# Kernel tuning notes

Hardware: AMD Instinct MI355X
Metric: run time of the kernel (lower is better)

The kernel has to match this reference:

```python
import jax, jax.numpy as jnp
import numpy as np

NP_, NA, NPR = 3000, 25, 1071
N = NP_ + NA + NPR          # 4096 total nodes
D = 256                     # latent_dim
H = 8                       # num_heads
DH = D // H                 # head dim 32
FF = 4 * D                  # feed-forward dim
BLOCKS = 3                  # args.block_num
E = 131072                  # edges = N * 32 avg degree
EPS = 1e-5


def setup_inputs() -> dict:
    key = jax.random.key(0)
    ks = jax.random.split(key, 16)
    s = 1.0 / np.sqrt(D)
    return {
        "adj_row": jax.random.randint(ks[0], (E,), 0, N, dtype=jnp.int32),
        "adj_col": jax.random.randint(ks[1], (E,), 0, N, dtype=jnp.int32),
        "adj_val": jax.random.uniform(ks[2], (E,), dtype=jnp.float32),
        "pe": jax.random.normal(ks[3], (NP_, D), dtype=jnp.float32) * s,
        "ae": jax.random.normal(ks[4], (NA, D), dtype=jnp.float32) * s,
        "qe": jax.random.normal(ks[5], (NPR, D), dtype=jnp.float32) * s,
        "Wqkv": jax.random.normal(ks[6], (D, 3 * D), dtype=jnp.float32) * s,
        "Wo": jax.random.normal(ks[7], (D, D), dtype=jnp.float32) * s,
        "W1": jax.random.normal(ks[8], (D, FF), dtype=jnp.float32) * s,
        "b1": jnp.zeros((FF,), dtype=jnp.float32),
        "W2": jax.random.normal(ks[9], (FF, D), dtype=jnp.float32) * (1.0 / np.sqrt(FF)),
        "b2": jnp.zeros((D,), dtype=jnp.float32),
        "ln1_g": jnp.ones((D,), dtype=jnp.float32),
        "ln1_b": jnp.zeros((D,), dtype=jnp.float32),
        "ln2_g": jnp.ones((D,), dtype=jnp.float32),
        "ln2_b": jnp.zeros((D,), dtype=jnp.float32),
    }


def _layer_norm(x, g, b):
    m = jnp.mean(x, axis=-1, keepdims=True)
    v = jnp.mean(jnp.square(x - m), axis=-1, keepdims=True)
    return (x - m) * jax.lax.rsqrt(v + EPS) * g + b


def _encoder_layer(x, Wqkv, Wo, W1, b1, W2, b2, ln1_g, ln1_b, ln2_g, ln2_b):
    # x: [N, D]; standard post-LN transformer encoder (dropout = 0)
    qkv = x @ Wqkv                                   # [N, 3D]
    q, k, v = jnp.split(qkv, 3, axis=-1)
    q = q.reshape(N, H, DH)
    k = k.reshape(N, H, DH)
    v = v.reshape(N, H, DH)
    scores = jnp.einsum("nhd,mhd->hnm", q, k) / np.sqrt(DH)  # [H, N, N]
    att = jax.nn.softmax(scores, axis=-1)
    o = jnp.einsum("hnm,mhd->nhd", att, v).reshape(N, D) @ Wo
    x = _layer_norm(x + o, ln1_g, ln1_b)
    h = jax.nn.relu(x @ W1 + b1) @ W2 + b2
    return _layer_norm(x + h, ln2_g, ln2_b)


def _spmm(adj_row, adj_col, adj_val, x):
    # sparse [N,N] @ dense [N,D] via gather + segment-sum scatter
    msgs = adj_val[:, None] * x[adj_col]             # [E, D]
    return jax.ops.segment_sum(msgs, adj_row, num_segments=N)


def reference(adj_row, adj_col, adj_val, pe, ae, qe, Wqkv, Wo, W1, b1, W2, b2,
              ln1_g, ln1_b, ln2_g, ln2_b):
    cur = jnp.concatenate([pe, ae, qe], axis=0)      # [N, D]
    total = cur
    for _ in range(BLOCKS):
        t = _spmm(adj_row, adj_col, adj_val, cur)
        t = _encoder_layer(t, Wqkv, Wo, W1, b1, W2, b2, ln1_g, ln1_b, ln2_g, ln2_b)
        cur = t + cur                                # residual per block
        total = total + cur                          # sum over embeds list
    protein = total[:NP_]
    aa = total[NP_:NP_ + NA]
    prop = total[NP_ + NA:]
    return total, protein, aa, prop
```

## Files before the change

### kernel.cpp

```cpp
#include <hip/hip_runtime.h>
#include <hip/hip_bf16.h>


#define NPROT 3000
#define NAA   25
#define NPROP 1071
#define NTOT  4096
#define DIM   256
#define NH    8
#define DHD   32
#define FFD   1024
#define NEDGE 131072
#define LNEPS 1e-5f
#define KSPLIT 4
#define KVQ (NTOT/KSPLIT)

typedef unsigned short u16;
typedef unsigned int u32;
typedef __attribute__((ext_vector_type(8))) short short8v;
typedef __attribute__((ext_vector_type(4))) float float4v;
typedef __attribute__((ext_vector_type(2))) unsigned int uint2v;

__device__ __forceinline__ u16 f2bu(float x){
  union { __hip_bfloat16 h; u16 u; } c; c.h = __float2bfloat16(x); return c.u;
}
__device__ __forceinline__ float bu2f(u16 u){
  union { u32 i; float f; } c; c.i = ((u32)u) << 16; return c.f;
}
__device__ __forceinline__ float4v mfma16(short8v a, short8v b, float4v c){
  return __builtin_amdgcn_mfma_f32_16x16x32_bf16(a, b, c, 0, 0, 0);
}
__device__ __forceinline__ u32 packbf(float lo, float hi){
  u32 ul = __builtin_bit_cast(u32, lo);
  u32 uh = __builtin_bit_cast(u32, hi);
  return (ul >> 16) | (uh & 0xFFFF0000u);
}
__device__ __forceinline__ void gload_lds16(const u16* g, u16* l){
  __builtin_amdgcn_global_load_lds(
      (const __attribute__((address_space(1))) void*)g,
      (__attribute__((address_space(3))) void*)l, 16, 0, 0);
}

__global__ __launch_bounds__(256) void k_embed(const float* __restrict__ pe, const float* __restrict__ ae,
                                               const float* __restrict__ qe,
                                               float* __restrict__ cur, float* __restrict__ tot,
                                               u16* __restrict__ curb){
  int i = blockIdx.x*256 + threadIdx.x;
  int row = i >> 8;
  float v;
  if (row < NPROT)           v = pe[i];
  else if (row < NPROT+NAA)  v = ae[i - NPROT*DIM];
  else                       v = qe[i - (NPROT+NAA)*DIM];
  cur[i] = v; tot[i] = v; curb[i] = f2bu(v);
}

__global__ __launch_bounds__(256) void k_zero(int* __restrict__ p, int n){
  int i = blockIdx.x*256 + threadIdx.x; if (i < n) p[i] = 0;
}

__global__ __launch_bounds__(256) void k_wconv_all(const float* __restrict__ Wqkv, const float* __restrict__ Wo,
                                                   const float* __restrict__ W1, const float* __restrict__ W2,
                                                   u16* __restrict__ wqkvt, u16* __restrict__ wot,
                                                   u16* __restrict__ w1t, u16* __restrict__ w2t){
  int b = blockIdx.x;
  const float* W; u16* Wt; int K, N, n;
  if (b < 768)       { W = Wqkv; Wt = wqkvt; K = 256;  N = 768;  n = b; }
  else if (b < 1024) { W = Wo;   Wt = wot;   K = 256;  N = 256;  n = b - 768; }
  else if (b < 2048) { W = W1;   Wt = w1t;   K = 256;  N = 1024; n = b - 1024; }
  else               { W = W2;   Wt = w2t;   K = 1024; N = 256;  n = b - 2048; }
  for (int k = threadIdx.x; k < K; k += 256)
    Wt[(size_t)n*K + k] = f2bu(W[(size_t)k*N + n]);
}

__global__ __launch_bounds__(256) void k_hist(const int* __restrict__ rows, int* __restrict__ cnt){
  int e = blockIdx.x*256 + threadIdx.x; if (e < NEDGE) atomicAdd(&cnt[rows[e]], 1);
}

__global__ __launch_bounds__(64) void k_scan(const int* __restrict__ cnt, int* __restrict__ rowptr,
                                             int* __restrict__ cursor){
  int lane = threadIdx.x;
  int sum = 0;
  for (int i = 0; i < 64; ++i) sum += cnt[lane*64 + i];
  int pref = sum;
  #pragma unroll
  for (int off = 1; off < 64; off <<= 1){
    int u = __shfl_up(pref, off);
    if (lane >= off) pref += u;
  }
  int run = pref - sum;
  for (int i = 0; i < 64; ++i){
    int c = cnt[lane*64 + i];
    rowptr[lane*64 + i] = run;
    cursor[lane*64 + i] = run;
    run += c;
  }
  if (lane == 63) rowptr[NTOT] = run;
}

__global__ __launch_bounds__(256) void k_scatter(const int* __restrict__ rows, const int* __restrict__ cols,
                                                 const float* __restrict__ vals, int* __restrict__ cursor,
                                                 int* __restrict__ ccol, float* __restrict__ cval){
  int e = blockIdx.x*256 + threadIdx.x; if (e >= NEDGE) return;
  int p = atomicAdd(&cursor[rows[e]], 1);
  ccol[p] = cols[e]; cval[p] = vals[e];
}

__global__ __launch_bounds__(256) void k_spmm(const int* __restrict__ rowptr, const int* __restrict__ ccol,
                                              const float* __restrict__ cval, const u16* __restrict__ xb,
                                              float* __restrict__ out, u16* __restrict__ outb){
  int r = blockIdx.x, c = threadIdx.x;
  int s = rowptr[r], e = rowptr[r+1];
  float acc = 0.f;
  for (int i = s; i < e; ++i)
    acc += cval[i] * bu2f(xb[((size_t)ccol[i] << 8) + c]);
  out[((size_t)r << 8) + c] = acc;
  outb[((size_t)r << 8) + c] = f2bu(acc);
}

template<int RELU, int BIAS, int BF16OUT>
__global__ __launch_bounds__(256) void k_gemm64(const u16* __restrict__ A, const u16* __restrict__ Wt,
                                                const float* __restrict__ bias, void* __restrict__ Cv,
                                                int M, int K, int Nc){
  __shared__ u16 Al[64*64];
  __shared__ u16 Bl[64*64];
  const int tid = threadIdx.x;
  const int w  = tid >> 6, l = tid & 63, lr = l & 15, g = l >> 4;
  const int row0 = blockIdx.y*64, col0 = blockIdx.x*64;
  const int wm = (w >> 1)*32, wn = (w & 1)*32;
  const int srow = (l >> 3);
  const int soct = (l & 7) ^ srow;
  float4v acc[2][2] = {};

  for (int k0 = 0; k0 < K; k0 += 64){
    #pragma unroll
    for (int i = 0; i < 2; ++i){
      int row = 16*w + 8*i + srow;
      gload_lds16(A  + (size_t)(row0 + row)*K + k0 + soct*8, Al + (16*w + 8*i)*64);
      gload_lds16(Wt + (size_t)(col0 + row)*K + k0 + soct*8, Bl + (16*w + 8*i)*64);
    }
    __syncthreads();
    #pragma unroll
    for (int kk = 0; kk < 2; ++kk){
      short8v af[2], bfr[2];
      #pragma unroll
      for (int i = 0; i < 2; ++i){
        int am = wm + 16*i + lr;
        af[i]  = *(const short8v*)(Al + am*64 + (((4*kk + g) ^ (am & 7))*8));
        int bn = wn + 16*i + lr;
        bfr[i] = *(const short8v*)(Bl + bn*64 + (((4*kk + g) ^ (bn & 7))*8));
      }
      acc[0][0] = mfma16(af[0], bfr[0], acc[0][0]);
      acc[0][1] = mfma16(af[0], bfr[1], acc[0][1]);
      acc[1][0] = mfma16(af[1], bfr[0], acc[1][0]);
      acc[1][1] = mfma16(af[1], bfr[1], acc[1][1]);
    }
    __syncthreads();
  }

  #pragma unroll
  for (int mi = 0; mi < 2; ++mi){
    #pragma unroll
    for (int ni = 0; ni < 2; ++ni){
      int col = col0 + wn + 16*ni + lr;
      float bv = BIAS ? bias[col] : 0.f;
      #pragma unroll
      for (int j = 0; j < 4; ++j){
        int row = row0 + wm + 16*mi + 4*g + j;
        float v = acc[mi][ni][j] + bv;
        if (RELU) v = fmaxf(v, 0.f);
        if (BF16OUT) ((u16*)Cv)[(size_t)row*Nc + col] = f2bu(v);
        else         ((float*)Cv)[(size_t)row*Nc + col] = v;
      }
    }
  }
}

__global__ __launch_bounds__(256) void k_attn_mfma(const u16* __restrict__ qbf,
                                                   u16* __restrict__ p0, u16* __restrict__ p1,
                                                   u16* __restrict__ p2, u16* __restrict__ p3,
                                                   float* __restrict__ mbuf, float* __restrict__ lbuf){
  __shared__ u16 Vt[2][32*64];
  __shared__ u16 Pl[4][16*64];
  __shared__ float Fl[4][16];
  const int h   = blockIdx.y;
  const int ks  = blockIdx.z;
  const int qb  = blockIdx.x * 128;
  const int tid = threadIdx.x;
  const int w   = tid >> 6;
  const int l   = tid & 63;
  const int lr  = l & 15;
  const int g   = l >> 4;
  const int sr  = tid >> 2;
  const int sq  = tid & 3;
  const float SC  = 0.17677669529663687f;
  const float SCL = 0.25503837f;
  const float DEFER = 31.368f;
  u16* opart = (ks == 0) ? p0 : (ks == 1) ? p1 : (ks == 2) ? p2 : p3;

  short8v qfA = *(const short8v*)(qbf + (size_t)(qb + 16*w + lr)*768 + h*DHD + 8*g);
  short8v qfB = *(const short8v*)(qbf + (size_t)(qb + 64 + 16*w + lr)*768 + h*DHD + 8*g);
  short8v ones;
  #pragma unroll
  for (int j = 0; j < 8; ++j) ones[j] = (short)0x3F80;

  float4v oaA0 = {0,0,0,0}, oaA1 = {0,0,0,0}, acclA = {0,0,0,0};
  float4v oaB0 = {0,0,0,0}, oaB1 = {0,0,0,0}, acclB = {0,0,0,0};
  float mrunA = -1e30f, mrunB = -1e30f;
  u16* pw = &Pl[w][0];

  const u16* vp = qbf + (size_t)(ks*KVQ + sr)*768 + 512 + h*DHD + 8*sq;
  const u16* kp = qbf + (size_t)(ks*KVQ + lr)*768 + 256 + h*DHD + 8*g;
  short8v vreg = *(const short8v*)vp;
  short8v kf0 = *(const short8v*)(kp);
  short8v kf1 = *(const short8v*)(kp + (size_t)16*768);
  short8v kf2 = *(const short8v*)(kp + (size_t)32*768);
  short8v kf3 = *(const short8v*)(kp + (size_t)48*768);

  const int gh = g >> 1, gl = 4*(g & 1);
  const int slotp0 = (0 + g) ^ (lr & 7);
  const int slotp1 = (4 + g) ^ (lr & 7);

  const int NIT = KVQ/64;
  for (int t = 0; t < NIT; ++t){
    u16* vt = &Vt[t & 1][0];
    #pragma unroll
    for (int j = 0; j < 8; ++j){
      int row  = 8*sq + j;
      int slot = (sr >> 3) ^ j;
      vt[row*64 + slot*8 + (sr & 7)] = (u16)vreg[j];
    }
    __syncthreads();
    vp += (size_t)64*768;
    vreg = *(const short8v*)vp;

    float4v sA0 = mfma16(kf0, qfA, (float4v){0,0,0,0});
    float4v sA1 = mfma16(kf1, qfA, (float4v){0,0,0,0});
    float4v sA2 = mfma16(kf2, qfA, (float4v){0,0,0,0});
    float4v sA3 = mfma16(kf3, qfA, (float4v){0,0,0,0});
    float4v sB0 = mfma16(kf0, qfB, (float4v){0,0,0,0});
    float4v sB1 = mfma16(kf1, qfB, (float4v){0,0,0,0});
    float4v sB2 = mfma16(kf2, qfB, (float4v){0,0,0,0});
    float4v sB3 = mfma16(kf3, qfB, (float4v){0,0,0,0});
    kp += (size_t)64*768;
    kf0 = *(const short8v*)(kp);
    kf1 = *(const short8v*)(kp + (size_t)16*768);
    kf2 = *(const short8v*)(kp + (size_t)32*768);
    kf3 = *(const short8v*)(kp + (size_t)48*768);

    short8v v00 = *(const short8v*)(vt + lr*64      + slotp0*8);
    short8v v10 = *(const short8v*)(vt + (lr+16)*64 + slotp0*8);
    short8v v01 = *(const short8v*)(vt + lr*64      + slotp1*8);
    short8v v11 = *(const short8v*)(vt + (lr+16)*64 + slotp1*8);

    {
      float m0 = fmaxf(fmaxf(fmaxf(sA0[0],sA0[1]),sA0[2]),sA0[3]);
      float m1 = fmaxf(fmaxf(fmaxf(sA1[0],sA1[1]),sA1[2]),sA1[3]);
      float m2 = fmaxf(fmaxf(fmaxf(sA2[0],sA2[1]),sA2[2]),sA2[3]);
      float m3 = fmaxf(fmaxf(fmaxf(sA3[0],sA3[1]),sA3[2]),sA3[3]);
      float tm = fmaxf(fmaxf(fmaxf(m0,m1),m2),m3);
      tm = fmaxf(tm, __shfl_xor(tm, 16));
      tm = fmaxf(tm, __shfl_xor(tm, 32));
      const bool nomax = __all(tm <= mrunA + DEFER);
      float fac = 1.f;
      if (!nomax){
        float mn = fmaxf(mrunA, tm);
        fac = exp2f((mrunA - mn)*SCL);
        mrunA = mn;
      }
      float mns = mrunA*SCL;
      #pragma unroll
      for (int j = 0; j < 4; ++j){
        sA0[j] = exp2f(__builtin_fmaf(sA0[j], SCL, -mns));
        sA1[j] = exp2f(__builtin_fmaf(sA1[j], SCL, -mns));
        sA2[j] = exp2f(__builtin_fmaf(sA2[j], SCL, -mns));
        sA3[j] = exp2f(__builtin_fmaf(sA3[j], SCL, -mns));
      }
      uint2v* d0 = (uint2v*)(pw + lr*64 + ((0 + gh) ^ (lr & 7))*8 + gl);
      uint2v* d1 = (uint2v*)(pw + lr*64 + ((2 + gh) ^ (lr & 7))*8 + gl);
      uint2v* d2 = (uint2v*)(pw + lr*64 + ((4 + gh) ^ (lr & 7))*8 + gl);
      uint2v* d3 = (uint2v*)(pw + lr*64 + ((6 + gh) ^ (lr & 7))*8 + gl);
      *d0 = (uint2v){packbf(sA0[0],sA0[1]), packbf(sA0[2],sA0[3])};
      *d1 = (uint2v){packbf(sA1[0],sA1[1]), packbf(sA1[2],sA1[3])};
      *d2 = (uint2v){packbf(sA2[0],sA2[1]), packbf(sA2[2],sA2[3])};
      *d3 = (uint2v){packbf(sA3[0],sA3[1]), packbf(sA3[2],sA3[3])};
      if (!nomax){
        if (g == 0) Fl[w][lr] = fac;
        float fq0 = Fl[w][4*g+0], fq1 = Fl[w][4*g+1], fq2 = Fl[w][4*g+2], fq3 = Fl[w][4*g+3];
        oaA0[0]*=fq0; oaA0[1]*=fq1; oaA0[2]*=fq2; oaA0[3]*=fq3;
        oaA1[0]*=fq0; oaA1[1]*=fq1; oaA1[2]*=fq2; oaA1[3]*=fq3;
        acclA[0]*=fq0; acclA[1]*=fq1; acclA[2]*=fq2; acclA[3]*=fq3;
      }
      short8v pa0 = *(const short8v*)(pw + lr*64 + slotp0*8);
      short8v pa1 = *(const short8v*)(pw + lr*64 + slotp1*8);
      oaA0  = mfma16(pa0, v00, oaA0);
      oaA1  = mfma16(pa0, v10, oaA1);
      acclA = mfma16(pa0, ones, acclA);
      oaA0  = mfma16(pa1, v01, oaA0);
      oaA1  = mfma16(pa1, v11, oaA1);
      acclA = mfma16(pa1, ones, acclA);
    }
    {
      float m0 = fmaxf(fmaxf(fmaxf(sB0[0],sB0[1]),sB0[2]),sB0[3]);
      float m1 = fmaxf(fmaxf(fmaxf(sB1[0],sB1[1]),sB1[2]),sB1[3]);
      float m2 = fmaxf(fmaxf(fmaxf(sB2[0],sB2[1]),sB2[2]),sB2[3]);
      float m3 = fmaxf(fmaxf(fmaxf(sB3[0],sB3[1]),sB3[2]),sB3[3]);
      float tm = fmaxf(fmaxf(fmaxf(m0,m1),m2),m3);
      tm = fmaxf(tm, __shfl_xor(tm, 16));
      tm = fmaxf(tm, __shfl_xor(tm, 32));
      const bool nomax = __all(tm <= mrunB + DEFER);
      float fac = 1.f;
      if (!nomax){
        float mn = fmaxf(mrunB, tm);
        fac = exp2f((mrunB - mn)*SCL);
        mrunB = mn;
      }
      float mns = mrunB*SCL;
      #pragma unroll
      for (int j = 0; j < 4; ++j){
        sB0[j] = exp2f(__builtin_fmaf(sB0[j], SCL, -mns));
        sB1[j] = exp2f(__builtin_fmaf(sB1[j], SCL, -mns));
        sB2[j] = exp2f(__builtin_fmaf(sB2[j], SCL, -mns));
        sB3[j] = exp2f(__builtin_fmaf(sB3[j], SCL, -mns));
      }
      uint2v* d0 = (uint2v*)(pw + lr*64 + ((0 + gh) ^ (lr & 7))*8 + gl);
      uint2v* d1 = (uint2v*)(pw + lr*64 + ((2 + gh) ^ (lr & 7))*8 + gl);
      uint2v* d2 = (uint2v*)(pw + lr*64 + ((4 + gh) ^ (lr & 7))*8 + gl);
      uint2v* d3 = (uint2v*)(pw + lr*64 + ((6 + gh) ^ (lr & 7))*8 + gl);
      *d0 = (uint2v){packbf(sB0[0],sB0[1]), packbf(sB0[2],sB0[3])};
      *d1 = (uint2v){packbf(sB1[0],sB1[1]), packbf(sB1[2],sB1[3])};
      *d2 = (uint2v){packbf(sB2[0],sB2[1]), packbf(sB2[2],sB2[3])};
      *d3 = (uint2v){packbf(sB3[0],sB3[1]), packbf(sB3[2],sB3[3])};
      if (!nomax){
        if (g == 0) Fl[w][lr] = fac;
        float fq0 = Fl[w][4*g+0], fq1 = Fl[w][4*g+1], fq2 = Fl[w][4*g+2], fq3 = Fl[w][4*g+3];
        oaB0[0]*=fq0; oaB0[1]*=fq1; oaB0[2]*=fq2; oaB0[3]*=fq3;
        oaB1[0]*=fq0; oaB1[1]*=fq1; oaB1[2]*=fq2; oaB1[3]*=fq3;
        acclB[0]*=fq0; acclB[1]*=fq1; acclB[2]*=fq2; acclB[3]*=fq3;
      }
      short8v pa0 = *(const short8v*)(pw + lr*64 + slotp0*8);
      short8v pa1 = *(const short8v*)(pw + lr*64 + slotp1*8);
      oaB0  = mfma16(pa0, v00, oaB0);
      oaB1  = mfma16(pa0, v10, oaB1);
      acclB = mfma16(pa0, ones, acclB);
      oaB0  = mfma16(pa1, v01, oaB0);
      oaB1  = mfma16(pa1, v11, oaB1);
      acclB = mfma16(pa1, ones, acclB);
    }
  }

  #pragma unroll
  for (int j = 0; j < 4; ++j){
    size_t rowA = (size_t)(qb + 16*w + 4*g + j);
    size_t rowB = rowA + 64;
    opart[rowA*DIM + h*DHD + lr]      = f2bu(oaA0[j]);
    opart[rowA*DIM + h*DHD + 16 + lr] = f2bu(oaA1[j]);
    opart[rowB*DIM + h*DHD + lr]      = f2bu(oaB0[j]);
    opart[rowB*DIM + h*DHD + 16 + lr] = f2bu(oaB1[j]);
  }
  if (l < 16){
    size_t miA = (size_t)(ks*NH + h)*NTOT + qb + 16*w + lr;
    mbuf[miA]      = mrunA*SC;
    mbuf[miA + 64] = mrunB*SC;
  }
  if (lr == 0){
    #pragma unroll
    for (int j = 0; j < 4; ++j){
      size_t miA = (size_t)(ks*NH + h)*NTOT + qb + 16*w + 4*g + j;
      lbuf[miA]      = acclA[j];
      lbuf[miA + 64] = acclB[j];
    }
  }
}

__global__ __launch_bounds__(256) void k_attn_merge4(const u16* __restrict__ p0, const u16* __restrict__ p1,
                                                     const u16* __restrict__ p2, const u16* __restrict__ p3,
                                                     const float* __restrict__ mbuf, const float* __restrict__ lbuf,
                                                     u16* __restrict__ obf){
  int i = blockIdx.x*256 + threadIdx.x;
  int r = i >> 8, c = i & 255, h = c >> 5;
  float m0 = mbuf[(size_t)(0*NH + h)*NTOT + r];
  float m1 = mbuf[(size_t)(1*NH + h)*NTOT + r];
  float m2 = mbuf[(size_t)(2*NH + h)*NTOT + r];
  float m3 = mbuf[(size_t)(3*NH + h)*NTOT + r];
  float M = fmaxf(fmaxf(m0, m1), fmaxf(m2, m3));
  float e0 = __expf(m0 - M), e1 = __expf(m1 - M);
  float e2 = __expf(m2 - M), e3 = __expf(m3 - M);
  float L = e0*lbuf[(size_t)(0*NH + h)*NTOT + r] + e1*lbuf[(size_t)(1*NH + h)*NTOT + r]
          + e2*lbuf[(size_t)(2*NH + h)*NTOT + r] + e3*lbuf[(size_t)(3*NH + h)*NTOT + r];
  float acc = e0*bu2f(p0[i]) + e1*bu2f(p1[i]) + e2*bu2f(p2[i]) + e3*bu2f(p3[i]);
  obf[i] = f2bu(acc / L);
}

template<int DUAL>
__global__ __launch_bounds__(256) void k_add_ln(const float* __restrict__ a, const float* __restrict__ b,
                                                const float* __restrict__ g, const float* __restrict__ be,
                                                float* __restrict__ out, u16* __restrict__ out2){
  __shared__ float red[4];
  int r = blockIdx.x, c = threadIdx.x;
  float v = a[((size_t)r << 8) + c] + b[((size_t)r << 8) + c];
  float s = v;
  #pragma unroll
  for (int off = 32; off; off >>= 1) s += __shfl_down(s, off);
  if ((c & 63) == 0) red[c >> 6] = s;
  __syncthreads();
  float mean = (red[0]+red[1]+red[2]+red[3]) * (1.f/DIM);
  __syncthreads();
  float d = v - mean;
  float s2 = d*d;
  #pragma unroll
  for (int off = 32; off; off >>= 1) s2 += __shfl_down(s2, off);
  if ((c & 63) == 0) red[c >> 6] = s2;
  __syncthreads();
  float var = (red[0]+red[1]+red[2]+red[3]) * (1.f/DIM);
  float rv = d * rsqrtf(var + LNEPS) * g[c] + be[c];
  out[((size_t)r << 8) + c] = rv;
  if (DUAL) out2[((size_t)r << 8) + c] = f2bu(rv);
}

template<int FINAL>
__global__ __launch_bounds__(256) void k_add_ln_upd(const float* __restrict__ a, const float* __restrict__ b,
                                                    const float* __restrict__ g, const float* __restrict__ be,
                                                    float* __restrict__ cur, float* __restrict__ tot,
                                                    u16* __restrict__ curb, float* __restrict__ out){
  __shared__ float red[4];
  int r = blockIdx.x, c = threadIdx.x;
  size_t idx = ((size_t)r << 8) + c;
  float v = a[idx] + b[idx];
  float s = v;
  #pragma unroll
  for (int off = 32; off; off >>= 1) s += __shfl_down(s, off);
  if ((c & 63) == 0) red[c >> 6] = s;
  __syncthreads();
  float mean = (red[0]+red[1]+red[2]+red[3]) * (1.f/DIM);
  __syncthreads();
  float d = v - mean;
  float s2 = d*d;
  #pragma unroll
  for (int off = 32; off; off >>= 1) s2 += __shfl_down(s2, off);
  if ((c & 63) == 0) red[c >> 6] = s2;
  __syncthreads();
  float var = (red[0]+red[1]+red[2]+red[3]) * (1.f/DIM);
  float rv = d * rsqrtf(var + LNEPS) * g[c] + be[c];
  float cu = cur[idx] + rv;
  cur[idx] = cu;
  if (!FINAL) curb[idx] = f2bu(cu);
  float tv = tot[idx] + cu;
  tot[idx] = tv;
  if (FINAL){
    out[idx] = tv;
    out[(size_t)NTOT*DIM + idx] = tv;
  }
}

extern "C" void kernel_launch(void* const* d_in, const int* in_sizes, int n_in,
                              void* d_out, int out_size, void* d_ws, size_t ws_size,
                              hipStream_t stream){
  const int*   adj_row = (const int*)  d_in[0];
  const int*   adj_col = (const int*)  d_in[1];
  const float* adj_val = (const float*)d_in[2];
  const float* pe   = (const float*)d_in[3];
  const float* ae   = (const float*)d_in[4];
  const float* qe   = (const float*)d_in[5];
  const float* Wqkv = (const float*)d_in[6];
  const float* Wo   = (const float*)d_in[7];
  const float* W1   = (const float*)d_in[8];
  const float* b1   = (const float*)d_in[9];
  const float* W2   = (const float*)d_in[10];
  const float* b2   = (const float*)d_in[11];
  const float* g1   = (const float*)d_in[12];
  const float* be1  = (const float*)d_in[13];
  const float* g2   = (const float*)d_in[14];
  const float* be2  = (const float*)d_in[15];
  float* out = (float*)d_out;

  char* w = (char*)d_ws;
  float* cur  = (float*)w; w += (size_t)NTOT*DIM*4;
  float* tot  = (float*)w; w += (size_t)NTOT*DIM*4;
  float* tf   = (float*)w; w += (size_t)NTOT*DIM*4;
  float* pbuf = (float*)w; w += (size_t)NTOT*DIM*4;
  float* x1   = (float*)w; w += (size_t)NTOT*DIM*4;
  u16* tbf    = (u16*)w;   w += (size_t)NTOT*DIM*2;
  u16* curb   = (u16*)w;   w += (size_t)NTOT*DIM*2;
  u16* x1b    = (u16*)w;   w += (size_t)NTOT*DIM*2;
  u16* hq     = (u16*)w;   w += (size_t)NTOT*FFD*2;
  u16* wqkvt  = (u16*)w;   w += (size_t)768*256*2;
  u16* wot    = (u16*)w;   w += (size_t)256*256*2;
  u16* w1t    = (u16*)w;   w += (size_t)1024*256*2;
  u16* w2t    = (u16*)w;   w += (size_t)256*1024*2;
  int* rowptr = (int*)w;   w += (size_t)(NTOT+1)*4;
  int* cnt    = (int*)w;   w += (size_t)NTOT*4;
  int* cursor = (int*)w;   w += (size_t)NTOT*4;
  int* ccol   = (int*)w;   w += (size_t)NEDGE*4;
  float* cval = (float*)w; w += (size_t)NEDGE*4;
  u16* qbf = hq;
  u16* obf = hq;
  u16* pp0 = (u16*)x1;
  u16* pp1 = (u16*)x1 + (size_t)NTOT*DIM;
  u16* pp2 = x1b;
  u16* pp3 = curb;
  float* mbuf = (float*)tbf;
  float* lbuf = mbuf + (size_t)KSPLIT*NH*NTOT;

  k_zero<<<16, 256, 0, stream>>>(cnt, NTOT);
  k_embed<<<NTOT, 256, 0, stream>>>(pe, ae, qe, cur, tot, curb);
  k_hist<<<NEDGE/256, 256, 0, stream>>>(adj_row, cnt);
  k_scan<<<1, 64, 0, stream>>>(cnt, rowptr, cursor);
  k_scatter<<<NEDGE/256, 256, 0, stream>>>(adj_row, adj_col, adj_val, cursor, ccol, cval);
  k_wconv_all<<<2304, 256, 0, stream>>>(Wqkv, Wo, W1, W2, wqkvt, wot, w1t, w2t);

  for (int blk = 0; blk < 3; ++blk){
    k_spmm<<<NTOT, 256, 0, stream>>>(rowptr, ccol, cval, curb, tf, tbf);
    k_gemm64<0,0,1><<<dim3(768/64, NTOT/64), 256, 0, stream>>>(tbf, wqkvt, nullptr, qbf, NTOT, 256, 768);
    k_attn_mfma<<<dim3(NTOT/128, NH, KSPLIT), 256, 0, stream>>>(qbf, pp0, pp1, pp2, pp3, mbuf, lbuf);
    k_attn_merge4<<<NTOT*DIM/256, 256, 0, stream>>>(pp0, pp1, pp2, pp3, mbuf, lbuf, obf);
    k_gemm64<0,0,0><<<dim3(256/64, NTOT/64), 256, 0, stream>>>(obf, wot, nullptr, pbuf, NTOT, 256, 256);
    k_add_ln<1><<<NTOT, 256, 0, stream>>>(tf, pbuf, g1, be1, x1, x1b);
    k_gemm64<1,1,1><<<dim3(1024/64, NTOT/64), 256, 0, stream>>>(x1b, w1t, b1, hq, NTOT, 256, 1024);
    k_gemm64<0,1,0><<<dim3(256/64, NTOT/64), 256, 0, stream>>>(hq, w2t, b2, pbuf, NTOT, 1024, 256);
    if (blk < 2)
      k_add_ln_upd<0><<<NTOT, 256, 0, stream>>>(x1, pbuf, g2, be2, cur, tot, curb, nullptr);
    else
      k_add_ln_upd<1><<<NTOT, 256, 0, stream>>>(x1, pbuf, g2, be2, cur, tot, nullptr, out);
  }
}
```

Measured before the change: 464.7 us.

## Process 256 queries per attention block to amortize K/V loads

Result: slower. 516.7 us (+11.2%).

```diff
diff --git a/kernel.cpp b/kernel.cpp
--- a/kernel.cpp
+++ b/kernel.cpp
@@ -184,7 +184,7 @@
   __shared__ float Fl[4][16];
   const int h   = blockIdx.y;
   const int ks  = blockIdx.z;
-  const int qb  = blockIdx.x * 128;
+  const int qb  = blockIdx.x * 256;
   const int tid = threadIdx.x;
   const int w   = tid >> 6;
   const int l   = tid & 63;
@@ -197,15 +197,23 @@
   const float DEFER = 31.368f;
   u16* opart = (ks == 0) ? p0 : (ks == 1) ? p1 : (ks == 2) ? p2 : p3;
 
-  short8v qfA = *(const short8v*)(qbf + (size_t)(qb + 16*w + lr)*768 + h*DHD + 8*g);
-  short8v qfB = *(const short8v*)(qbf + (size_t)(qb + 64 + 16*w + lr)*768 + h*DHD + 8*g);
+  short8v qf[4];
+  #pragma unroll
+  for (int ss = 0; ss < 4; ++ss)
+    qf[ss] = *(const short8v*)(qbf + (size_t)(qb + 64*ss + 16*w + lr)*768 + h*DHD + 8*g);
   short8v ones;
   #pragma unroll
   for (int j = 0; j < 8; ++j) ones[j] = (short)0x3F80;
 
-  float4v oaA0 = {0,0,0,0}, oaA1 = {0,0,0,0}, acclA = {0,0,0,0};
-  float4v oaB0 = {0,0,0,0}, oaB1 = {0,0,0,0}, acclB = {0,0,0,0};
-  float mrunA = -1e30f, mrunB = -1e30f;
+  float4v oa0[4], oa1[4], accl[4];
+  float mrun[4];
+  #pragma unroll
+  for (int ss = 0; ss < 4; ++ss){
+    oa0[ss] = (float4v){0,0,0,0};
+    oa1[ss] = (float4v){0,0,0,0};
+    accl[ss] = (float4v){0,0,0,0};
+    mrun[ss] = -1e30f;
+  }
   u16* pw = &Pl[w][0];
 
   const u16* vp = qbf + (size_t)(ks*KVQ + sr)*768 + 512 + h*DHD + 8*sq;
@@ -233,14 +241,14 @@
     vp += (size_t)64*768;
     vreg = *(const short8v*)vp;
 
-    float4v sA0 = mfma16(kf0, qfA, (float4v){0,0,0,0});
-    float4v sA1 = mfma16(kf1, qfA, (float4v){0,0,0,0});
-    float4v sA2 = mfma16(kf2, qfA, (float4v){0,0,0,0});
-    float4v sA3 = mfma16(kf3, qfA, (float4v){0,0,0,0});
-    float4v sB0 = mfma16(kf0, qfB, (float4v){0,0,0,0});
-    float4v sB1 = mfma16(kf1, qfB, (float4v){0,0,0,0});
-    float4v sB2 = mfma16(kf2, qfB, (float4v){0,0,0,0});
-    float4v sB3 = mfma16(kf3, qfB, (float4v){0,0,0,0});
+    float4v sv[4][4];
+    #pragma unroll
+    for (int ss = 0; ss < 4; ++ss){
+      sv[ss][0] = mfma16(kf0, qf[ss], (float4v){0,0,0,0});
+      sv[ss][1] = mfma16(kf1, qf[ss], (float4v){0,0,0,0});
+      sv[ss][2] = mfma16(kf2, qf[ss], (float4v){0,0,0,0});
+      sv[ss][3] = mfma16(kf3, qf[ss], (float4v){0,0,0,0});
+    }
     kp += (size_t)64*768;
     kf0 = *(const short8v*)(kp);
     kf1 = *(const short8v*)(kp + (size_t)16*768);
@@ -252,122 +260,80 @@
     short8v v01 = *(const short8v*)(vt + lr*64      + slotp1*8);
     short8v v11 = *(const short8v*)(vt + (lr+16)*64 + slotp1*8);
 
-    {
-      float m0 = fmaxf(fmaxf(fmaxf(sA0[0],sA0[1]),sA0[2]),sA0[3]);
-      float m1 = fmaxf(fmaxf(fmaxf(sA1[0],sA1[1]),sA1[2]),sA1[3]);
-      float m2 = fmaxf(fmaxf(fmaxf(sA2[0],sA2[1]),sA2[2]),sA2[3]);
-      float m3 = fmaxf(fmaxf(fmaxf(sA3[0],sA3[1]),sA3[2]),sA3[3]);
+    #pragma unroll
+    for (int ss = 0; ss < 4; ++ss){
+      float m0 = fmaxf(fmaxf(fmaxf(sv[ss][0][0],sv[ss][0][1]),sv[ss][0][2]),sv[ss][0][3]);
+      float m1 = fmaxf(fmaxf(fmaxf(sv[ss][1][0],sv[ss][1][1]),sv[ss][1][2]),sv[ss][1][3]);
+      float m2 = fmaxf(fmaxf(fmaxf(sv[ss][2][0],sv[ss][2][1]),sv[ss][2][2]),sv[ss][2][3]);
+      float m3 = fmaxf(fmaxf(fmaxf(sv[ss][3][0],sv[ss][3][1]),sv[ss][3][2]),sv[ss][3][3]);
       float tm = fmaxf(fmaxf(fmaxf(m0,m1),m2),m3);
       tm = fmaxf(tm, __shfl_xor(tm, 16));
       tm = fmaxf(tm, __shfl_xor(tm, 32));
-      const bool nomax = __all(tm <= mrunA + DEFER);
+      const bool nomax = __all(tm <= mrun[ss] + DEFER);
       float fac = 1.f;
       if (!nomax){
-        float mn = fmaxf(mrunA, tm);
-        fac = exp2f((mrunA - mn)*SCL);
-        mrunA = mn;
-      }
-      float mns = mrunA*SCL;
+        float mn = fmaxf(mrun[ss], tm);
+        fac = exp2f((mrun[ss] - mn)*SCL);
+        mrun[ss] = mn;
+      }
+      float mns = mrun[ss]*SCL;
       #pragma unroll
-      for (int j = 0; j < 4; ++j){
-        sA0[j] = exp2f(__builtin_fmaf(sA0[j], SCL, -mns));
-        sA1[j] = exp2f(__builtin_fmaf(sA1[j], SCL, -mns));
-        sA2[j] = exp2f(__builtin_fmaf(sA2[j], SCL, -mns));
-        sA3[j] = exp2f(__builtin_fmaf(sA3[j], SCL, -mns));
+      for (int i = 0; i < 4; ++i){
+        sv[ss][i][0] = exp2f(__builtin_fmaf(sv[ss][i][0], SCL, -mns));
+        sv[ss][i][1] = exp2f(__builtin_fmaf(sv[ss][i][1], SCL, -mns));
+        sv[ss][i][2] = exp2f(__builtin_fmaf(sv[ss][i][2], SCL, -mns));
+        sv[ss][i][3] = exp2f(__builtin_fmaf(sv[ss][i][3], SCL, -mns));
       }
       uint2v* d0 = (uint2v*)(pw + lr*64 + ((0 + gh) ^ (lr & 7))*8 + gl);
       uint2v* d1 = (uint2v*)(pw + lr*64 + ((2 + gh) ^ (lr & 7))*8 + gl);
       uint2v* d2 = (uint2v*)(pw + lr*64 + ((4 + gh) ^ (lr & 7))*8 + gl);
       uint2v* d3 = (uint2v*)(pw + lr*64 + ((6 + gh) ^ (lr & 7))*8 + gl);
-      *d0 = (uint2v){packbf(sA0[0],sA0[1]), packbf(sA0[2],sA0[3])};
-      *d1 = (uint2v){packbf(sA1[0],sA1[1]), packbf(sA1[2],sA1[3])};
-      *d2 = (uint2v){packbf(sA2[0],sA2[1]), packbf(sA2[2],sA2[3])};
-      *d3 = (uint2v){packbf(sA3[0],sA3[1]), packbf(sA3[2],sA3[3])};
+      *d0 = (uint2v){packbf(sv[ss][0][0],sv[ss][0][1]), packbf(sv[ss][0][2],sv[ss][0][3])};
+      *d1 = (uint2v){packbf(sv[ss][1][0],sv[ss][1][1]), packbf(sv[ss][1][2],sv[ss][1][3])};
+      *d2 = (uint2v){packbf(sv[ss][2][0],sv[ss][2][1]), packbf(sv[ss][2][2],sv[ss][2][3])};
+      *d3 = (uint2v){packbf(sv[ss][3][0],sv[ss][3][1]), packbf(sv[ss][3][2],sv[ss][3][3])};
       if (!nomax){
         if (g == 0) Fl[w][lr] = fac;
         float fq0 = Fl[w][4*g+0], fq1 = Fl[w][4*g+1], fq2 = Fl[w][4*g+2], fq3 = Fl[w][4*g+3];
-        oaA0[0]*=fq0; oaA0[1]*=fq1; oaA0[2]*=fq2; oaA0[3]*=fq3;
-        oaA1[0]*=fq0; oaA1[1]*=fq1; oaA1[2]*=fq2; oaA1[3]*=fq3;
-        acclA[0]*=fq0; acclA[1]*=fq1; acclA[2]*=fq2; acclA[3]*=fq3;
+        oa0[ss][0]*=fq0; oa0[ss][1]*=fq1; oa0[ss][2]*=fq2; oa0[ss][3]*=fq3;
+        oa1[ss][0]*=fq0; oa1[ss][1]*=fq1; oa1[ss][2]*=fq2; oa1[ss][3]*=fq3;
+        accl[ss][0]*=fq0; accl[ss][1]*=fq1; accl[ss][2]*=fq2; accl[ss][3]*=fq3;
       }
       short8v pa0 = *(const short8v*)(pw + lr*64 + slotp0*8);
       short8v pa1 = *(const short8v*)(pw + lr*64 + slotp1*8);
-      oaA0  = mfma16(pa0, v00, oaA0);
-      oaA1  = mfma16(pa0, v10, oaA1);
-      acclA = mfma16(pa0, ones, acclA);
-      oaA0  = mfma16(pa1, v01, oaA0);
-      oaA1  = mfma16(pa1, v11, oaA1);
-      acclA = mfma16(pa1, ones, acclA);
-    }
-    {
-      float m0 = fmaxf(fmaxf(fmaxf(sB0[0],sB0[1]),sB0[2]),sB0[3]);
-      float m1 = fmaxf(fmaxf(fmaxf(sB1[0],sB1[1]),sB1[2]),sB1[3]);
-      float m2 = fmaxf(fmaxf(fmaxf(sB2[0],sB2[1]),sB2[2]),sB2[3]);
-      float m3 = fmaxf(fmaxf(fmaxf(sB3[0],sB3[1]),sB3[2]),sB3[3]);
-      float tm = fmaxf(fmaxf(fmaxf(m0,m1),m2),m3);
-      tm = fmaxf(tm, __shfl_xor(tm, 16));
-      tm = fmaxf(tm, __shfl_xor(tm, 32));
-      const bool nomax = __all(tm <= mrunB + DEFER);
-      float fac = 1.f;
-      if (!nomax){
-        float mn = fmaxf(mrunB, tm);
-        fac = exp2f((mrunB - mn)*SCL);
-        mrunB = mn;
-      }
-      float mns = mrunB*SCL;
+      oa0[ss]  = mfma16(pa0, v00, oa0[ss]);
+      oa1[ss]  = mfma16(pa0, v10, oa1[ss]);
+      accl[ss] = mfma16(pa0, ones, accl[ss]);
+      oa0[ss]  = mfma16(pa1, v01, oa0[ss]);
+      oa1[ss]  = mfma16(pa1, v11, oa1[ss]);
+      accl[ss] = mfma16(pa1, ones, accl[ss]);
+    }
+  }
+
+  #pragma unroll
+  for (int ss = 0; ss < 4; ++ss){
+    #pragma unroll
+    for (int j = 0; j < 4; ++j){
+      size_t row = (size_t)(qb + 64*ss + 16*w + 4*g + j);
+      opart[row*DIM + h*DHD + lr]      = f2bu(oa0[ss][j]);
+      opart[row*DIM + h*DHD + 16 + lr] = f2bu(oa1[ss][j]);
+    }
+  }
+  if (l < 16){
+    #pragma unroll
+    for (int ss = 0; ss < 4; ++ss){
+      size_t mi = (size_t)(ks*NH + h)*NTOT + qb + 64*ss + 16*w + lr;
+      mbuf[mi] = mrun[ss]*SC;
+    }
+  }
+  if (lr == 0){
+    #pragma unroll
+    for (int ss = 0; ss < 4; ++ss){
       #pragma unroll
       for (int j = 0; j < 4; ++j){
-        sB0[j] = exp2f(__builtin_fmaf(sB0[j], SCL, -mns));
-        sB1[j] = exp2f(__builtin_fmaf(sB1[j], SCL, -mns));
-        sB2[j] = exp2f(__builtin_fmaf(sB2[j], SCL, -mns));
-        sB3[j] = exp2f(__builtin_fmaf(sB3[j], SCL, -mns));
-      }
-      uint2v* d0 = (uint2v*)(pw + lr*64 + ((0 + gh) ^ (lr & 7))*8 + gl);
-      uint2v* d1 = (uint2v*)(pw + lr*64 + ((2 + gh) ^ (lr & 7))*8 + gl);
-      uint2v* d2 = (uint2v*)(pw + lr*64 + ((4 + gh) ^ (lr & 7))*8 + gl);
-      uint2v* d3 = (uint2v*)(pw + lr*64 + ((6 + gh) ^ (lr & 7))*8 + gl);
-      *d0 = (uint2v){packbf(sB0[0],sB0[1]), packbf(sB0[2],sB0[3])};
-      *d1 = (uint2v){packbf(sB1[0],sB1[1]), packbf(sB1[2],sB1[3])};
-      *d2 = (uint2v){packbf(sB2[0],sB2[1]), packbf(sB2[2],sB2[3])};
-      *d3 = (uint2v){packbf(sB3[0],sB3[1]), packbf(sB3[2],sB3[3])};
-      if (!nomax){
-        if (g == 0) Fl[w][lr] = fac;
-        float fq0 = Fl[w][4*g+0], fq1 = Fl[w][4*g+1], fq2 = Fl[w][4*g+2], fq3 = Fl[w][4*g+3];
-        oaB0[0]*=fq0; oaB0[1]*=fq1; oaB0[2]*=fq2; oaB0[3]*=fq3;
-        oaB1[0]*=fq0; oaB1[1]*=fq1; oaB1[2]*=fq2; oaB1[3]*=fq3;
-        acclB[0]*=fq0; acclB[1]*=fq1; acclB[2]*=fq2; acclB[3]*=fq3;
-      }
-      short8v pa0 = *(const short8v*)(pw + lr*64 + slotp0*8);
-      short8v pa1 = *(const short8v*)(pw + lr*64 + slotp1*8);
-      oaB0  = mfma16(pa0, v00, oaB0);
-      oaB1  = mfma16(pa0, v10, oaB1);
-      acclB = mfma16(pa0, ones, acclB);
-      oaB0  = mfma16(pa1, v01, oaB0);
-      oaB1  = mfma16(pa1, v11, oaB1);
-      acclB = mfma16(pa1, ones, acclB);
-    }
-  }
-
-  #pragma unroll
-  for (int j = 0; j < 4; ++j){
-    size_t rowA = (size_t)(qb + 16*w + 4*g + j);
-    size_t rowB = rowA + 64;
-    opart[rowA*DIM + h*DHD + lr]      = f2bu(oaA0[j]);
-    opart[rowA*DIM + h*DHD + 16 + lr] = f2bu(oaA1[j]);
-    opart[rowB*DIM + h*DHD + lr]      = f2bu(oaB0[j]);
-    opart[rowB*DIM + h*DHD + 16 + lr] = f2bu(oaB1[j]);
-  }
-  if (l < 16){
-    size_t miA = (size_t)(ks*NH + h)*NTOT + qb + 16*w + lr;
-    mbuf[miA]      = mrunA*SC;
-    mbuf[miA + 64] = mrunB*SC;
-  }
-  if (lr == 0){
-    #pragma unroll
-    for (int j = 0; j < 4; ++j){
-      size_t miA = (size_t)(ks*NH + h)*NTOT + qb + 16*w + 4*g + j;
-      lbuf[miA]      = acclA[j];
-      lbuf[miA + 64] = acclB[j];
+        size_t mi = (size_t)(ks*NH + h)*NTOT + qb + 64*ss + 16*w + 4*g + j;
+        lbuf[mi] = accl[ss][j];
+      }
     }
   }
 }
@@ -511,7 +477,7 @@
   for (int blk = 0; blk < 3; ++blk){
     k_spmm<<<NTOT, 256, 0, stream>>>(rowptr, ccol, cval, curb, tf, tbf);
     k_gemm64<0,0,1><<<dim3(768/64, NTOT/64), 256, 0, stream>>>(tbf, wqkvt, nullptr, qbf, NTOT, 256, 768);
-    k_attn_mfma<<<dim3(NTOT/128, NH, KSPLIT), 256, 0, stream>>>(qbf, pp0, pp1, pp2, pp3, mbuf, lbuf);
+    k_attn_mfma<<<dim3(NTOT/256, NH, KSPLIT), 256, 0, stream>>>(qbf, pp0, pp1, pp2, pp3, mbuf, lbuf);
     k_attn_merge4<<<NTOT*DIM/256, 256, 0, stream>>>(pp0, pp1, pp2, pp3, mbuf, lbuf, obf);
     k_gemm64<0,0,0><<<dim3(256/64, NTOT/64), 256, 0, stream>>>(obf, wot, nullptr, pbuf, NTOT, 256, 256);
     k_add_ln<1><<<NTOT, 256, 0, stream>>>(tf, pbuf, g1, be1, x1, x1b);
```
